# Optimization experiments

Hardware: AMD Instinct MI355X
Metric: run time of the kernel (lower is better)

The kernel has to match this reference:

```python
import jax, jax.numpy as jnp
import numpy as np

EPS = 1e-05


def setup_inputs() -> dict:
    key = jax.random.key(0)
    k0, k1, k2, k3, k4 = jax.random.split(key, 5)
    B, N, D = 8, 4096, 1024
    scale = 1.0 / np.sqrt(D)  # roughly xavier scale for D x D
    return {
        "x": jax.random.normal(k0, (B, N, D), dtype=jnp.float32),
        "w_query_real": jax.random.normal(k1, (D, D), dtype=jnp.float32) * scale,
        "w_query_imag": jax.random.normal(k2, (D, D), dtype=jnp.float32) * scale,
        "w_key": jax.random.normal(k3, (D, D), dtype=jnp.float32) * scale,
        "w_value": jax.random.normal(k4, (D, D), dtype=jnp.float32) * scale,
    }


def reference(x, w_query_real, w_query_imag, w_key, w_value):
    # x is real -> x_real = x_imag = x (torch fallback branch)
    q_real = jnp.einsum('bnd,de->bne', x, w_query_real)
    q_imag = jnp.einsum('bnd,de->bne', x, w_query_imag)
    query = jax.nn.relu(q_real) * jax.nn.relu(q_imag)  # relu gating; dropout p=0

    key = jnp.einsum('bnd,de->bne', x, w_key)
    value = jnp.einsum('bnd,de->bne', x, w_value)
    # L2 norm over the sequence axis (dim=1), keepdim
    key = key / (jnp.linalg.norm(key, axis=1, keepdims=True) + EPS)
    value = value / (jnp.linalg.norm(value, axis=1, keepdims=True) + EPS)

    kv_attn = jax.nn.relu(jnp.einsum('bnd,bne->bde', key, value))  # [B, D, D]
    return jnp.einsum('bnd,bde->bne', query, kv_attn)
```

## Files before the change

kernel.cpp:

```cpp
#include <hip/hip_runtime.h>
#include <stdint.h>
#include <stddef.h>

#define D_ 1024
#define NSEQ_ 4096
#define BATCH_ 8
#define BN_ (BATCH_ * NSEQ_)

typedef __attribute__((ext_vector_type(8))) short short8;
typedef __attribute__((ext_vector_type(4))) short short4_t;
typedef __attribute__((ext_vector_type(4))) float float4_t;

__device__ __forceinline__ short f2b(float f) {
  union { float f; uint32_t u; } x; x.f = f;
  uint32_t r = x.u + 0x7fffu + ((x.u >> 16) & 1u);
  return (short)(r >> 16);
}
__device__ __forceinline__ float b2f(short s) {
  union { float f; uint32_t u; } x; x.u = ((uint32_t)(uint16_t)s) << 16; return x.f;
}

__device__ __forceinline__ void gll16(const void* g, void* l) {
  auto gp = reinterpret_cast<const uint32_t __attribute__((address_space(1)))*>(
      reinterpret_cast<uintptr_t>(g));
  auto lp = reinterpret_cast<uint32_t __attribute__((address_space(3)))*>(
      reinterpret_cast<uintptr_t>(l));
  __builtin_amdgcn_global_load_lds(gp, lp, 16, 0, 0);
}

#define MFMA16(a, b, c) __builtin_amdgcn_mfma_f32_16x16x32_bf16(a, b, c, 0, 0, 0)

__global__ void convert_x(const float* __restrict__ X, short* __restrict__ Xb) {
  const size_t i = (size_t)blockIdx.x * 256 + threadIdx.x;
  const float4_t* p = (const float4_t*)(X + i * 8);
  float4_t a = p[0], b = p[1];
  short8 o;
  o[0] = f2b(a.x); o[1] = f2b(a.y); o[2] = f2b(a.z); o[3] = f2b(a.w);
  o[4] = f2b(b.x); o[5] = f2b(b.y); o[6] = f2b(b.z); o[7] = f2b(b.w);
  *(short8*)(Xb + i * 8) = o;
}

__global__ void transpose_convert_w(const float* __restrict__ w0, const float* __restrict__ w1,
                                    const float* __restrict__ w2, const float* __restrict__ w3,
                                    short* __restrict__ wT) {
  __shared__ float tile[32][33];
  const int z = blockIdx.z;
  const float* src = (z == 0) ? w0 : (z == 1) ? w1 : (z == 2) ? w2 : w3;
  short* dst = wT + (size_t)z * D_ * D_;
  const int d0 = blockIdx.y * 32, e0 = blockIdx.x * 32;
  const int tx = threadIdx.x, ty = threadIdx.y;
#pragma unroll
  for (int i = 0; i < 4; ++i) {
    int d = ty + i * 8;
    tile[d][tx] = src[(size_t)(d0 + d) * D_ + (e0 + tx)];
  }
  __syncthreads();
#pragma unroll
  for (int i = 0; i < 4; ++i) {
    int e = ty + i * 8;
    dst[(size_t)(e0 + e) * D_ + (d0 + tx)] = f2b(tile[tx][e]);
  }
}

__global__ __launch_bounds__(256, 2) void gemm_x4w(
    const short* __restrict__ Xb, const short* __restrict__ Wall,
    short* __restrict__ qout, short* __restrict__ kT, short* __restrict__ vT,
    float* __restrict__ ssk, float* __restrict__ ssv) {
  __shared__ union {
    struct { short As[128 * 32]; short Bs[4 * 64 * 32]; } s;
    short T[64 * 136];
  } u;

  const int t = threadIdx.x;
  const int w = t >> 6;
  const int lane = t & 63;
  const int l16 = lane & 15;
  const int quad = lane >> 4;
  const int wm = w >> 1, wn = w & 1;
  const int M0 = blockIdx.y * 128;
  const int E0 = blockIdx.x * 64;

  const float4_t fz = {0.f, 0.f, 0.f, 0.f};
  float4_t acc[4][4][2];
#pragma unroll
  for (int a = 0; a < 4; ++a)
#pragma unroll
    for (int i = 0; i < 4; ++i)
#pragma unroll
      for (int j = 0; j < 2; ++j) acc[a][i][j] = fz;

  const int rowq = lane >> 2;
  const int chunk = (lane & 3) * 8;

  for (int k0 = 0; k0 < 1024; k0 += 32) {
#pragma unroll
    for (int r = 0; r < 6; ++r) {
      const int q = w * 6 + r;
      if (q < 8) {
        gll16(Xb + (size_t)(M0 + q * 16 + rowq) * 1024 + (k0 + chunk), &u.s.As[q * 512]);
      } else {
        const int qq = q - 8;
        gll16(Wall + (size_t)(qq >> 2) * D_ * D_ +
                  (size_t)(E0 + (qq & 3) * 16 + rowq) * 1024 + (k0 + chunk),
              &u.s.Bs[qq * 512]);
      }
    }
    __syncthreads();
    short8 aF[4], bF[4][2];
#pragma unroll
    for (int i = 0; i < 4; ++i)
      aF[i] = *(const short8*)&u.s.As[(wm * 64 + i * 16 + l16) * 32 + quad * 8];
#pragma unroll
    for (int wt = 0; wt < 4; ++wt)
#pragma unroll
      for (int j = 0; j < 2; ++j)
        bF[wt][j] = *(const short8*)&u.s.Bs[wt * 2048 + (wn * 32 + j * 16 + l16) * 32 + quad * 8];
#pragma unroll
    for (int i = 0; i < 4; ++i)
#pragma unroll
      for (int wt = 0; wt < 4; ++wt)
#pragma unroll
        for (int j = 0; j < 2; ++j)
          acc[wt][i][j] = MFMA16(aF[i], bF[wt][j], acc[wt][i][j]);
    __syncthreads();
  }

#pragma unroll
  for (int i = 0; i < 4; ++i) {
    const int rowb = M0 + wm * 64 + i * 16 + quad * 4;
#pragma unroll
    for (int j = 0; j < 2; ++j) {
      const int col = E0 + wn * 32 + j * 16 + l16;
#pragma unroll
      for (int rr = 0; rr < 4; ++rr) {
        float v = fmaxf(acc[0][i][j][rr], 0.f) * fmaxf(acc[1][i][j][rr], 0.f);
        qout[(size_t)(rowb + rr) * 1024 + col] = f2b(v);
      }
    }
  }

  const int b = M0 >> 12;
  const int n0 = M0 & 4095;
#pragma unroll
  for (int wt = 2; wt < 4; ++wt) {
    short* dst = (wt == 2) ? kT : vT;
    float* ss = (wt == 2) ? ssk : ssv;
    if (wt == 3) __syncthreads();
#pragma unroll
    for (int i = 0; i < 4; ++i) {
      const int rowl = wm * 64 + i * 16 + quad * 4;
#pragma unroll
      for (int j = 0; j < 2; ++j) {
        const int coll = wn * 32 + j * 16 + l16;
#pragma unroll
        for (int rr = 0; rr < 4; ++rr)
          u.T[coll * 136 + rowl + rr] = f2b(acc[wt][i][j][rr]);
      }
    }
    __syncthreads();
#pragma unroll
    for (int it = 0; it < 4; ++it) {
      const int e = it * 16 + (t >> 4);
      const int mchunk = (t & 15) * 8;
      short8 vv = *(const short8*)&u.T[e * 136 + mchunk];
      *(short8*)&dst[((size_t)b * 1024 + E0 + e) * 4096 + n0 + mchunk] = vv;
      float s = 0.f;
#pragma unroll
      for (int x2 = 0; x2 < 8; ++x2) { float f = b2f(vv[x2]); s += f * f; }
      s += __shfl_xor(s, 1, 16);
      s += __shfl_xor(s, 2, 16);
      s += __shfl_xor(s, 4, 16);
      s += __shfl_xor(s, 8, 16);
      if ((t & 15) == 0) atomicAdd(&ss[b * 1024 + E0 + e], s);
    }
  }
}

__global__ void finish_norms(const float* __restrict__ ss, float* __restrict__ inv) {
  const int i = blockIdx.x * 256 + threadIdx.x;
  if (i < 2 * BATCH_ * D_) inv[i] = 1.f / (sqrtf(ss[i]) + 1e-5f);
}

__global__ __launch_bounds__(256, 2) void gemm_bt(
    const short* __restrict__ A, const short* __restrict__ Bm,
    size_t sAb, size_t sBb, int K, int mode,
    const float* __restrict__ rsb, const float* __restrict__ csb,
    void* __restrict__ outp) {
  __shared__ short As[128 * 32];
  __shared__ short Bs[128 * 32];
  const int t = threadIdx.x;
  const int w = t >> 6;
  const int lane = t & 63;
  const int l16 = lane & 15;
  const int quad = lane >> 4;
  const int wm = w >> 1, wn = w & 1;
  const int M0 = blockIdx.y * 128, N0 = blockIdx.x * 128, b = blockIdx.z;
  const short* Ab = A + (size_t)b * sAb;
  const short* Bb = Bm + (size_t)b * sBb;

  const float4_t fz = {0.f, 0.f, 0.f, 0.f};
  float4_t acc[4][4];
#pragma unroll
  for (int i = 0; i < 4; ++i)
#pragma unroll
    for (int j = 0; j < 4; ++j) acc[i][j] = fz;

  const int rowq = lane >> 2;
  const int chunk = (lane & 3) * 8;

  for (int k0 = 0; k0 < K; k0 += 32) {
#pragma unroll
    for (int r = 0; r < 4; ++r) {
      const int q = w * 4 + r;
      if (q < 8) {
        const int row = q * 16 + rowq;
        gll16(Ab + (size_t)(M0 + row) * K + (k0 + chunk), &As[q * 512]);
      } else {
        const int row = (q - 8) * 16 + rowq;
        gll16(Bb + (size_t)(N0 + row) * K + (k0 + chunk), &Bs[(q - 8) * 512]);
      }
    }
    __syncthreads();
    short8 aF[4], bF[4];
#pragma unroll
    for (int i = 0; i < 4; ++i)
      aF[i] = *(const short8*)&As[(wm * 64 + i * 16 + l16) * 32 + quad * 8];
#pragma unroll
    for (int j = 0; j < 4; ++j)
      bF[j] = *(const short8*)&Bs[(wn * 64 + j * 16 + l16) * 32 + quad * 8];
#pragma unroll
    for (int i = 0; i < 4; ++i)
#pragma unroll
      for (int j = 0; j < 4; ++j) acc[i][j] = MFMA16(aF[i], bF[j], acc[i][j]);
    __syncthreads();
  }

  if (mode == 0) {
    short* ob = (short*)outp + (size_t)b * D_ * D_;
    const float* rs = rsb + b * D_ + M0;
    const float* cs = csb + b * D_ + N0;
#pragma unroll
    for (int i = 0; i < 4; ++i) {
      const int rl = wm * 64 + i * 16 + quad * 4;
#pragma unroll
      for (int j = 0; j < 4; ++j) {
        const int cl = wn * 64 + j * 16 + l16;
        const float csc = cs[cl];
#pragma unroll
        for (int rr = 0; rr < 4; ++rr) {
          float v = acc[i][j][rr] * rs[rl + rr] * csc;
          v = fmaxf(v, 0.f);
          ob[(size_t)(M0 + rl + rr) * 1024 + (N0 + cl)] = f2b(v);
        }
      }
    }
  } else {
    float* of = (float*)outp + (size_t)b * NSEQ_ * D_;
#pragma unroll
    for (int i = 0; i < 4; ++i) {
      const int rl = wm * 64 + i * 16 + quad * 4;
#pragma unroll
      for (int j = 0; j < 4; ++j) {
        const int cl = wn * 64 + j * 16 + l16;
#pragma unroll
        for (int rr = 0; rr < 4; ++rr)
          of[(size_t)(M0 + rl + rr) * 1024 + (N0 + cl)] = acc[i][j][rr];
      }
    }
  }
}

extern "C" void kernel_launch(void* const* d_in, const int* in_sizes, int n_in,
                              void* d_out, int out_size, void* d_ws, size_t ws_size,
                              hipStream_t stream) {
  const float* x = (const float*)d_in[0];
  const float* wqr = (const float*)d_in[1];
  const float* wqi = (const float*)d_in[2];
  const float* wk = (const float*)d_in[3];
  const float* wv = (const float*)d_in[4];

  short* wT = (short*)d_ws;
  short* qb = wT + (size_t)4 * D_ * D_;
  short* kT = qb + (size_t)BN_ * D_;
  short* vT = kT + (size_t)BATCH_ * D_ * NSEQ_;
  short* kvT = vT + (size_t)BATCH_ * D_ * NSEQ_;
  float* ssk = (float*)(kvT + (size_t)BATCH_ * D_ * D_);
  float* ssv = ssk + BATCH_ * D_;
  float* invk = ssv + BATCH_ * D_;
  float* invv = invk + BATCH_ * D_;

  short* xb = (short*)d_out;

  hipMemsetAsync(ssk, 0, (size_t)2 * BATCH_ * D_ * sizeof(float), stream);

  convert_x<<<dim3(16384), 256, 0, stream>>>(x, xb);

  transpose_convert_w<<<dim3(32, 32, 4), dim3(32, 8), 0, stream>>>(wqr, wqi, wk, wv, wT);

  gemm_x4w<<<dim3(16, 256), 256, 0, stream>>>(xb, wT, qb, kT, vT, ssk, ssv);

  finish_norms<<<dim3(64), 256, 0, stream>>>(ssk, invk);

  gemm_bt<<<dim3(8, 8, 8), 256, 0, stream>>>(
      vT, kT, (size_t)D_ * NSEQ_, (size_t)D_ * NSEQ_, 4096, 0, invv, invk, (void*)kvT);

  gemm_bt<<<dim3(8, 32, 8), 256, 0, stream>>>(
      qb, kvT, (size_t)NSEQ_ * D_, (size_t)D_ * D_, 1024, 1, nullptr, nullptr, d_out);
}
```

Measured before the change: 778.6 us.

## Rewrite fused projection GEMM with 256x256 tiles, 4-stage LDS ring and interleaved weights

The four projection weights are interleaved in 16-row groups, so one 256-wide B tile carries all four projections for 64 output columns. The fused projection GEMM now uses 512 threads and 256x256 tiles. It loads through a 4-deep LDS ring with prefetch two steps ahead, swizzled LDS addressing to avoid bank conflicts, split MFMA phases with setprio, and a remapped block order for L2 locality. This targets the per-step sync stalls and low arithmetic intensity of the old 128x64x4 tiling, at the cost of 128KB of LDS, which limits occupancy, plus heavier register pressure.

Measured after the change: 764.1 us. No clear change (-1.9%).

```diff
diff --git a/kernel.cpp b/kernel.cpp
--- a/kernel.cpp
+++ b/kernel.cpp
@@ -46,7 +46,6 @@
   __shared__ float tile[32][33];
   const int z = blockIdx.z;
   const float* src = (z == 0) ? w0 : (z == 1) ? w1 : (z == 2) ? w2 : w3;
-  short* dst = wT + (size_t)z * D_ * D_;
   const int d0 = blockIdx.y * 32, e0 = blockIdx.x * 32;
   const int tx = threadIdx.x, ty = threadIdx.y;
 #pragma unroll
@@ -58,120 +57,169 @@
 #pragma unroll
   for (int i = 0; i < 4; ++i) {
     int e = ty + i * 8;
-    dst[(size_t)(e0 + e) * D_ + (d0 + tx)] = f2b(tile[tx][e]);
-  }
-}
-
-__global__ __launch_bounds__(256, 2) void gemm_x4w(
-    const short* __restrict__ Xb, const short* __restrict__ Wall,
+    const int eg = e0 + e;
+    const int row = ((eg >> 4) << 6) + (z << 4) + (eg & 15);
+    wT[(size_t)row * D_ + (d0 + tx)] = f2b(tile[tx][e]);
+  }
+}
+
+__global__ __launch_bounds__(512, 2) void gemm_x4w(
+    const short* __restrict__ Xb, const short* __restrict__ Wint,
     short* __restrict__ qout, short* __restrict__ kT, short* __restrict__ vT,
     float* __restrict__ ssk, float* __restrict__ ssv) {
-  __shared__ union {
-    struct { short As[128 * 32]; short Bs[4 * 64 * 32]; } s;
-    short T[64 * 136];
-  } u;
+  __shared__ short ring[4 * 16384];
 
   const int t = threadIdx.x;
   const int w = t >> 6;
   const int lane = t & 63;
   const int l16 = lane & 15;
   const int quad = lane >> 4;
-  const int wm = w >> 1, wn = w & 1;
-  const int M0 = blockIdx.y * 128;
-  const int E0 = blockIdx.x * 64;
+  const int wm = w >> 2;
+  const int wn = w & 3;
+
+  const int bid = blockIdx.x;
+  const int lin = (bid & 7) * 256 + (bid >> 3);
+  const int mt = lin >> 4;
+  const int nt = lin & 15;
+  const int M0 = mt * 256;
+  const int N0 = nt * 256;
+  const int E0 = nt * 64;
 
   const float4_t fz = {0.f, 0.f, 0.f, 0.f};
-  float4_t acc[4][4][2];
-#pragma unroll
-  for (int a = 0; a < 4; ++a)
+  float4_t acc[8][4];
+#pragma unroll
+  for (int i = 0; i < 8; ++i)
+#pragma unroll
+    for (int j = 0; j < 4; ++j) acc[i][j] = fz;
+
+  size_t goffA[2], goffB[2];
+  int ldsu[2];
+#pragma unroll
+  for (int r = 0; r < 2; ++r) {
+    const int uu = w * 2 + r;
+    const int row = uu * 16 + (lane >> 2);
+    const int sp = (lane & 3) ^ ((row >> 1) & 3);
+    goffA[r] = (size_t)(M0 + row) * 1024 + sp * 8;
+    goffB[r] = (size_t)(N0 + row) * 1024 + sp * 8;
+    ldsu[r] = uu * 512;
+  }
+  int aoff[8], boff[4];
+#pragma unroll
+  for (int i = 0; i < 8; ++i) {
+    const int row = wm * 128 + i * 16 + l16;
+    aoff[i] = row * 32 + ((quad ^ ((row >> 1) & 3)) << 3);
+  }
+#pragma unroll
+  for (int j = 0; j < 4; ++j) {
+    const int row = wn * 64 + j * 16 + l16;
+    boff[j] = row * 32 + ((quad ^ ((row >> 1) & 3)) << 3);
+  }
+
+#pragma unroll
+  for (int r = 0; r < 2; ++r) gll16(Xb + goffA[r], ring + ldsu[r]);
+#pragma unroll
+  for (int r = 0; r < 2; ++r) gll16(Wint + goffB[r], ring + 8192 + ldsu[r]);
+#pragma unroll
+  for (int r = 0; r < 2; ++r) gll16(Xb + goffA[r] + 32, ring + 16384 + ldsu[r]);
+#pragma unroll
+  for (int r = 0; r < 2; ++r) gll16(Wint + goffB[r] + 32, ring + 16384 + 8192 + ldsu[r]);
+  asm volatile("s_waitcnt vmcnt(4)" ::: "memory");
+  __builtin_amdgcn_s_barrier();
+
+#pragma unroll 1
+  for (int tt = 0; tt < 32; ++tt) {
+    const short* As = ring + (tt & 3) * 16384;
+    const short* Bs = As + 8192;
+    short8 aF[8], bF[4];
+
+#pragma unroll
+    for (int i = 0; i < 4; ++i) aF[i] = *(const short8*)&As[aoff[i]];
+#pragma unroll
+    for (int j = 0; j < 4; ++j) bF[j] = *(const short8*)&Bs[boff[j]];
+    if (tt < 30) {
+      short* dA = ring + ((tt + 2) & 3) * 16384;
+      const int k0 = (tt + 2) * 32;
+#pragma unroll
+      for (int r = 0; r < 2; ++r) gll16(Xb + goffA[r] + k0, dA + ldsu[r]);
+    }
+    __builtin_amdgcn_s_barrier();
+    asm volatile("s_waitcnt lgkmcnt(0)" ::: "memory");
+    __builtin_amdgcn_s_setprio(1);
 #pragma unroll
     for (int i = 0; i < 4; ++i)
 #pragma unroll
-      for (int j = 0; j < 2; ++j) acc[a][i][j] = fz;
-
-  const int rowq = lane >> 2;
-  const int chunk = (lane & 3) * 8;
-
-  for (int k0 = 0; k0 < 1024; k0 += 32) {
-#pragma unroll
-    for (int r = 0; r < 6; ++r) {
-      const int q = w * 6 + r;
-      if (q < 8) {
-        gll16(Xb + (size_t)(M0 + q * 16 + rowq) * 1024 + (k0 + chunk), &u.s.As[q * 512]);
-      } else {
-        const int qq = q - 8;
-        gll16(Wall + (size_t)(qq >> 2) * D_ * D_ +
-                  (size_t)(E0 + (qq & 3) * 16 + rowq) * 1024 + (k0 + chunk),
-              &u.s.Bs[qq * 512]);
-      }
-    }
-    __syncthreads();
-    short8 aF[4], bF[4][2];
-#pragma unroll
-    for (int i = 0; i < 4; ++i)
-      aF[i] = *(const short8*)&u.s.As[(wm * 64 + i * 16 + l16) * 32 + quad * 8];
-#pragma unroll
-    for (int wt = 0; wt < 4; ++wt)
-#pragma unroll
-      for (int j = 0; j < 2; ++j)
-        bF[wt][j] = *(const short8*)&u.s.Bs[wt * 2048 + (wn * 32 + j * 16 + l16) * 32 + quad * 8];
-#pragma unroll
-    for (int i = 0; i < 4; ++i)
-#pragma unroll
-      for (int wt = 0; wt < 4; ++wt)
-#pragma unroll
-        for (int j = 0; j < 2; ++j)
-          acc[wt][i][j] = MFMA16(aF[i], bF[wt][j], acc[wt][i][j]);
-    __syncthreads();
-  }
-
-#pragma unroll
-  for (int i = 0; i < 4; ++i) {
-    const int rowb = M0 + wm * 64 + i * 16 + quad * 4;
-#pragma unroll
-    for (int j = 0; j < 2; ++j) {
-      const int col = E0 + wn * 32 + j * 16 + l16;
-#pragma unroll
-      for (int rr = 0; rr < 4; ++rr) {
-        float v = fmaxf(acc[0][i][j][rr], 0.f) * fmaxf(acc[1][i][j][rr], 0.f);
-        qout[(size_t)(rowb + rr) * 1024 + col] = f2b(v);
-      }
-    }
-  }
-
+      for (int j = 0; j < 4; ++j) acc[i][j] = MFMA16(aF[i], bF[j], acc[i][j]);
+    __builtin_amdgcn_s_setprio(0);
+    __builtin_amdgcn_s_barrier();
+
+#pragma unroll
+    for (int i = 4; i < 8; ++i) aF[i] = *(const short8*)&As[aoff[i]];
+    if (tt < 30) {
+      short* dB = ring + ((tt + 2) & 3) * 16384 + 8192;
+      const int k0 = (tt + 2) * 32;
+#pragma unroll
+      for (int r = 0; r < 2; ++r) gll16(Wint + goffB[r] + k0, dB + ldsu[r]);
+    }
+    __builtin_amdgcn_s_barrier();
+    asm volatile("s_waitcnt lgkmcnt(0)" ::: "memory");
+    __builtin_amdgcn_s_setprio(1);
+#pragma unroll
+    for (int i = 4; i < 8; ++i)
+#pragma unroll
+      for (int j = 0; j < 4; ++j) acc[i][j] = MFMA16(aF[i], bF[j], acc[i][j]);
+    __builtin_amdgcn_s_setprio(0);
+    if (tt < 30) {
+      asm volatile("s_waitcnt vmcnt(4)" ::: "memory");
+    } else if (tt == 30) {
+      asm volatile("s_waitcnt vmcnt(0)" ::: "memory");
+    }
+    __builtin_amdgcn_s_barrier();
+  }
+
+  const int e = E0 + wn * 16 + l16;
+#pragma unroll
+  for (int i = 0; i < 8; ++i) {
+    const int rowg = M0 + wm * 128 + i * 16 + quad * 4;
+#pragma unroll
+    for (int rr = 0; rr < 4; ++rr) {
+      float v = fmaxf(acc[i][0][rr], 0.f) * fmaxf(acc[i][1][rr], 0.f);
+      qout[(size_t)(rowg + rr) * 1024 + e] = f2b(v);
+    }
+  }
+
+  short* T = ring;
   const int b = M0 >> 12;
   const int n0 = M0 & 4095;
 #pragma unroll
   for (int wt = 2; wt < 4; ++wt) {
     short* dst = (wt == 2) ? kT : vT;
     float* ss = (wt == 2) ? ssk : ssv;
-    if (wt == 3) __syncthreads();
-#pragma unroll
-    for (int i = 0; i < 4; ++i) {
-      const int rowl = wm * 64 + i * 16 + quad * 4;
-#pragma unroll
-      for (int j = 0; j < 2; ++j) {
-        const int coll = wn * 32 + j * 16 + l16;
-#pragma unroll
-        for (int rr = 0; rr < 4; ++rr)
-          u.T[coll * 136 + rowl + rr] = f2b(acc[wt][i][j][rr]);
-      }
-    }
     __syncthreads();
 #pragma unroll
+    for (int i = 0; i < 8; ++i) {
+      const int nl = wm * 128 + i * 16 + quad * 4;
+      const int el = wn * 16 + l16;
+      short4_t pk;
+#pragma unroll
+      for (int rr = 0; rr < 4; ++rr) pk[rr] = f2b(acc[i][wt][rr]);
+      *(short4_t*)&T[el * 264 + nl] = pk;
+    }
+    __syncthreads();
+#pragma unroll
     for (int it = 0; it < 4; ++it) {
-      const int e = it * 16 + (t >> 4);
-      const int mchunk = (t & 15) * 8;
-      short8 vv = *(const short8*)&u.T[e * 136 + mchunk];
-      *(short8*)&dst[((size_t)b * 1024 + E0 + e) * 4096 + n0 + mchunk] = vv;
+      const int ee = it * 16 + (t >> 5);
+      const int nch = (t & 31) * 8;
+      short8 vv = *(const short8*)&T[ee * 264 + nch];
+      *(short8*)&dst[((size_t)b * 1024 + E0 + ee) * 4096 + n0 + nch] = vv;
       float s = 0.f;
 #pragma unroll
       for (int x2 = 0; x2 < 8; ++x2) { float f = b2f(vv[x2]); s += f * f; }
-      s += __shfl_xor(s, 1, 16);
-      s += __shfl_xor(s, 2, 16);
-      s += __shfl_xor(s, 4, 16);
-      s += __shfl_xor(s, 8, 16);
-      if ((t & 15) == 0) atomicAdd(&ss[b * 1024 + E0 + e], s);
+      s += __shfl_xor(s, 1, 32);
+      s += __shfl_xor(s, 2, 32);
+      s += __shfl_xor(s, 4, 32);
+      s += __shfl_xor(s, 8, 32);
+      s += __shfl_xor(s, 16, 32);
+      if ((t & 31) == 0) atomicAdd(&ss[b * 1024 + E0 + ee], s);
     }
   }
 }
@@ -297,7 +345,7 @@
 
   transpose_convert_w<<<dim3(32, 32, 4), dim3(32, 8), 0, stream>>>(wqr, wqi, wk, wv, wT);
 
-  gemm_x4w<<<dim3(16, 256), 256, 0, stream>>>(xb, wT, qb, kT, vT, ssk, ssv);
+  gemm_x4w<<<dim3(2048), 512, 0, stream>>>(xb, wT, qb, kT, vT, ssk, ssv);
 
   finish_norms<<<dim3(64), 256, 0, stream>>>(ssk, invk);
 
```
